# Performance work log

Measured on AMD Instinct MI355X. Metric: run time of the kernel, lower is better.

## Reference

```python
import jax, jax.numpy as jnp
import numpy as np

N_NODES = 100000
N_EDGES = 3200000
N_GRAPHS = 1000

def setup_inputs() -> dict:
    key = jax.random.key(0)
    ks = jax.random.split(key, 8)
    x = jax.random.normal(ks[0], (N_NODES, 4), dtype=jnp.float32)
    edge_index = jax.random.randint(ks[1], (2, N_EDGES), 0, N_NODES, dtype=jnp.int64)
    batch = jnp.sort(jax.random.randint(ks[2], (N_NODES,), 0, N_GRAPHS, dtype=jnp.int64))
    def glorot(k, shape):
        lim = np.sqrt(6.0 / (shape[0] + shape[1]))
        return jax.random.uniform(k, shape, jnp.float32, -lim, lim)
    return {
        'x': x, 'edge_index': edge_index, 'batch': batch,
        'W1': glorot(ks[3], (4, 16)),  'b1': jnp.zeros((16,), jnp.float32),
        'W2': glorot(ks[4], (16, 16)), 'b2': jnp.zeros((16,), jnp.float32),
        'W3': glorot(ks[5], (16, 16)), 'b3': jnp.zeros((16,), jnp.float32),
        'lin_w': glorot(ks[6], (16, 1)), 'lin_b': jnp.zeros((1,), jnp.float32),
    }

def _gcn_norm(edge_index, num_nodes):
    # PyG GCNConv default: add self-loops, symmetric normalization
    loop = jnp.arange(num_nodes, dtype=edge_index.dtype)
    row = jnp.concatenate([edge_index[0], loop])  # source
    col = jnp.concatenate([edge_index[1], loop])  # target
    ones = jnp.ones(row.shape[0], dtype=jnp.float32)
    deg = jax.ops.segment_sum(ones, col, num_segments=num_nodes)
    dinv = jnp.where(deg > 0, jax.lax.rsqrt(deg), 0.0)
    norm = dinv[row] * dinv[col]  # [E+N]
    return row, col, norm

def _gcn_conv(x, row, col, norm, W, b, num_nodes):
    h = x @ W                                   # small GEMM first (fewer msg bytes)
    msg = h[row] * norm[:, None]                # gather + scale
    out = jax.ops.segment_sum(msg, col, num_segments=num_nodes)  # scatter-add
    return out + b

def reference(x, edge_index, batch, W1, b1, W2, b2, W3, b3, lin_w, lin_b):
    n = x.shape[0]
    row, col, norm = _gcn_norm(edge_index, n)
    h = _gcn_conv(x, row, col, norm, W1, b1, n)
    h = _gcn_conv(h, row, col, norm, W2, b2, n)
    h = _gcn_conv(h, row, col, norm, W3, b3, n)
    # global_mean_pool
    sums = jax.ops.segment_sum(h, batch, num_segments=N_GRAPHS)
    cnt = jax.ops.segment_sum(jnp.ones((n,), jnp.float32), batch, num_segments=N_GRAPHS)
    pooled = sums / jnp.maximum(cnt, 1.0)[:, None]
    # dropout p=0.5 is identity in eval mode
    logits = pooled @ lin_w + lin_b
    return jax.nn.sigmoid(logits)
```

## Files before the change

kernel.cpp:

```cpp
#include <hip/hip_runtime.h>
#include <math.h>


#define SHIFT      8
#define BSZ        256
#define NB_SCAT    128
#define B_SCAT     256
#define B_GATH     512
#define ROWMASK    0x1FFFFu
#define PSLOTS     64

__global__ void hist_kernel(const int* __restrict__ col, int E, int tile, int nbuck,
                            unsigned* __restrict__ M,
                            const float* __restrict__ W1, const float* __restrict__ b1,
                            const float* __restrict__ W2, const float* __restrict__ b2,
                            const float* __restrict__ W3, const float* __restrict__ b3,
                            const float* __restrict__ lin_w, const float* __restrict__ lin_b,
                            float* __restrict__ coeff,
                            float* __restrict__ sums, float* __restrict__ cnt, int ngraphs) {
    extern __shared__ unsigned h[];
    __shared__ float w3l[16], w2l[16];
    int t = threadIdx.x;
    for (int i = t; i < nbuck; i += blockDim.x) h[i] = 0;
    if (blockIdx.x == 0) {
        for (int i = t; i < ngraphs; i += blockDim.x) { sums[i] = 0.f; cnt[i] = 0.f; }
        if (t < 16) {
            float s = 0.f;
            for (int j = 0; j < 16; ++j) s += W3[t * 16 + j] * lin_w[j];
            w3l[t] = s;
        }
    }
    __syncthreads();
    if (blockIdx.x == 0 && t < 16) {
        float s = 0.f;
        for (int j = 0; j < 16; ++j) s += W2[t * 16 + j] * w3l[j];
        w2l[t] = s;
    }
    __syncthreads();
    if (blockIdx.x == 0) {
        if (t < 4) {
            float s = 0.f;
            for (int j = 0; j < 16; ++j) s += W1[t * 16 + j] * w2l[j];
            coeff[t] = s;
        } else if (t == 4) {
            float s = 0.f;
            for (int j = 0; j < 16; ++j) s += b1[j] * w2l[j];
            coeff[4] = s;
        } else if (t == 5) {
            float s = 0.f;
            for (int j = 0; j < 16; ++j) s += b2[j] * w3l[j];
            coeff[5] = s;
        } else if (t == 6) {
            float s = 0.f;
            for (int j = 0; j < 16; ++j) s += b3[j] * lin_w[j];
            coeff[6] = s;
        } else if (t == 7) {
            coeff[7] = lin_b[0];
        }
    }
    int b = blockIdx.x;
    int s = b * tile, e = min(s + tile, E);
    if (s < e) {
        int nq = (e - s) >> 2;
        const int4* c4 = (const int4*)(col + s);
        for (int q = t; q < nq; q += blockDim.x) {
            int4 c = c4[q];
            atomicAdd(&h[((unsigned)c.x) >> SHIFT], 1u);
            atomicAdd(&h[((unsigned)c.y) >> SHIFT], 1u);
            atomicAdd(&h[((unsigned)c.z) >> SHIFT], 1u);
            atomicAdd(&h[((unsigned)c.w) >> SHIFT], 1u);
        }
        for (int k = s + (nq << 2) + t; k < e; k += blockDim.x)
            atomicAdd(&h[((unsigned)col[k]) >> SHIFT], 1u);
    }
    __syncthreads();
    for (int i = t; i < nbuck; i += blockDim.x)
        M[(size_t)b * nbuck + i] = h[i];
}

__global__ void scanA_kernel(unsigned* __restrict__ M, unsigned* __restrict__ binTotal,
                             int nbuck) {
    __shared__ unsigned sc[NB_SCAT];
    int b = blockIdx.x;
    int t = threadIdx.x;
    unsigned v = M[(size_t)t * nbuck + b];
    sc[t] = v;
    __syncthreads();
    for (int off = 1; off < NB_SCAT; off <<= 1) {
        unsigned u = (t >= off) ? sc[t - off] : 0u;
        __syncthreads();
        sc[t] += u;
        __syncthreads();
    }
    M[(size_t)t * nbuck + b] = sc[t] - v;
    if (t == NB_SCAT - 1) binTotal[b] = sc[t];
}

__global__ void scatter_kernel(const int* __restrict__ row, const int* __restrict__ col,
                               int E, int tile, int nbuck,
                               const unsigned* __restrict__ M,
                               const unsigned* __restrict__ binTotal,
                               unsigned* __restrict__ bstart,
                               unsigned* __restrict__ out) {
    extern __shared__ unsigned lds[];
    unsigned* bb   = lds;
    unsigned* base = lds + nbuck;
    unsigned* tsum = lds + 2 * nbuck;
    int t = threadIdx.x;
    const int C = (2048 + B_SCAT - 1) / B_SCAT;
    unsigned lv[C];
    unsigned ls = 0;
    for (int k = 0; k < C; ++k) {
        int i = t * C + k;
        unsigned x = (i < nbuck) ? binTotal[i] : 0u;
        lv[k] = ls; ls += x;
    }
    tsum[t] = ls;
    __syncthreads();
    for (int off = 1; off < B_SCAT; off <<= 1) {
        unsigned u = (t >= off) ? tsum[t - off] : 0u;
        __syncthreads();
        tsum[t] += u;
        __syncthreads();
    }
    unsigned ex = (t == 0) ? 0u : tsum[t - 1];
    for (int k = 0; k < C; ++k) {
        int i = t * C + k;
        if (i < nbuck) bb[i] = ex + lv[k];
    }
    __syncthreads();
    int j = blockIdx.x;
    for (int i = t; i < nbuck; i += blockDim.x)
        base[i] = bb[i] + M[(size_t)j * nbuck + i];
    if (j == 0) {
        for (int i = t; i < nbuck; i += blockDim.x) bstart[i] = bb[i];
        if (t == 0) bstart[nbuck] = (unsigned)E;
    }
    __syncthreads();
    int s = j * tile, e = min(s + tile, E);
    if (s < e) {
        int nq = (e - s) >> 2;
        const int4* r4 = (const int4*)(row + s);
        const int4* c4 = (const int4*)(col + s);
        for (int q = t; q < nq; q += blockDim.x) {
            int4 r = r4[q];
            int4 c = c4[q];
            unsigned p0 = atomicAdd(&base[((unsigned)c.x) >> SHIFT], 1u);
            unsigned p1 = atomicAdd(&base[((unsigned)c.y) >> SHIFT], 1u);
            unsigned p2 = atomicAdd(&base[((unsigned)c.z) >> SHIFT], 1u);
            unsigned p3 = atomicAdd(&base[((unsigned)c.w) >> SHIFT], 1u);
            out[p0] = (unsigned)r.x | (((unsigned)c.x & (BSZ - 1)) << 17);
            out[p1] = (unsigned)r.y | (((unsigned)c.y & (BSZ - 1)) << 17);
            out[p2] = (unsigned)r.z | (((unsigned)c.z & (BSZ - 1)) << 17);
            out[p3] = (unsigned)r.w | (((unsigned)c.w & (BSZ - 1)) << 17);
        }
        for (int k = s + (nq << 2) + t; k < e; k += blockDim.x) {
            unsigned c = (unsigned)col[k];
            unsigned pos = atomicAdd(&base[c >> SHIFT], 1u);
            out[pos] = (unsigned)row[k] | ((c & (BSZ - 1)) << 17);
        }
    }
}

__global__ void degnode0_kernel(const unsigned* __restrict__ buck,
                                const unsigned* __restrict__ bstart,
                                const float* __restrict__ x, const float* __restrict__ coeff,
                                float* __restrict__ dinv, float* __restrict__ g, int n) {
    __shared__ float acc[BSZ];
    int b = blockIdx.x;
    if (threadIdx.x < BSZ) acc[threadIdx.x] = 0.f;
    __syncthreads();
    unsigned s = bstart[b], e = bstart[b + 1];
    unsigned sa = (s + 3u) & ~3u;
    if (sa > e) sa = e;
    if (s + threadIdx.x < sa)
        atomicAdd(&acc[buck[s + threadIdx.x] >> 17], 1.0f);
    unsigned nq = (e - sa) >> 2;
    const uint4* bq = (const uint4*)(buck + sa);
    for (unsigned q = threadIdx.x; q < nq; q += blockDim.x) {
        uint4 w = bq[q];
        atomicAdd(&acc[w.x >> 17], 1.0f);
        atomicAdd(&acc[w.y >> 17], 1.0f);
        atomicAdd(&acc[w.z >> 17], 1.0f);
        atomicAdd(&acc[w.w >> 17], 1.0f);
    }
    for (unsigned k = sa + (nq << 2) + threadIdx.x; k < e; k += blockDim.x)
        atomicAdd(&acc[buck[k] >> 17], 1.0f);
    __syncthreads();
    int node = b * BSZ + threadIdx.x;
    if (threadIdx.x < BSZ && node < n) {
        float d = rsqrtf(acc[threadIdx.x] + 1.0f);
        dinv[node] = d;
        float4 xv = ((const float4*)x)[node];
        float t0 = xv.x * coeff[0] + xv.y * coeff[1] + xv.z * coeff[2] + xv.w * coeff[3];
        g[node] = d * t0;
    }
}

__global__ void gather_kernel(const unsigned* __restrict__ buck,
                              const unsigned* __restrict__ bstart,
                              const float* __restrict__ dinv, const float* __restrict__ gin,
                              float* __restrict__ gout, const float* __restrict__ coeff,
                              int sidx, int n) {
    __shared__ float acc[BSZ];
    int b = blockIdx.x;
    if (threadIdx.x < BSZ) acc[threadIdx.x] = 0.f;
    __syncthreads();
    unsigned s = bstart[b], e = bstart[b + 1];
    unsigned sa = (s + 3u) & ~3u;
    if (sa > e) sa = e;
    if (s + threadIdx.x < sa) {
        unsigned w = buck[s + threadIdx.x];
        atomicAdd(&acc[w >> 17], gin[w & ROWMASK]);
    }
    unsigned nq = (e - sa) >> 2;
    const uint4* bq = (const uint4*)(buck + sa);
    for (unsigned q = threadIdx.x; q < nq; q += blockDim.x) {
        uint4 w = bq[q];
        float a0 = gin[w.x & ROWMASK];
        float a1 = gin[w.y & ROWMASK];
        float a2 = gin[w.z & ROWMASK];
        float a3 = gin[w.w & ROWMASK];
        atomicAdd(&acc[w.x >> 17], a0);
        atomicAdd(&acc[w.y >> 17], a1);
        atomicAdd(&acc[w.z >> 17], a2);
        atomicAdd(&acc[w.w >> 17], a3);
    }
    for (unsigned k = sa + (nq << 2) + threadIdx.x; k < e; k += blockDim.x) {
        unsigned w = buck[k];
        atomicAdd(&acc[w >> 17], gin[w & ROWMASK]);
    }
    __syncthreads();
    int node = b * BSZ + threadIdx.x;
    if (threadIdx.x < BSZ && node < n) {
        float d = dinv[node];
        float t = d * (acc[threadIdx.x] + gin[node]) + coeff[sidx];
        gout[node] = d * t;
    }
}

__global__ void gatherpool_kernel(const unsigned* __restrict__ buck,
                                  const unsigned* __restrict__ bstart,
                                  const float* __restrict__ dinv, const float* __restrict__ gin,
                                  const float* __restrict__ coeff, const int* __restrict__ batch,
                                  float* __restrict__ sums, float* __restrict__ cnt, int n) {
    __shared__ float acc[BSZ];
    __shared__ float ls[PSLOTS], lc[PSLOTS];
    __shared__ int bF;
    int b = blockIdx.x;
    if (threadIdx.x < BSZ) acc[threadIdx.x] = 0.f;
    for (int i = threadIdx.x; i < PSLOTS; i += blockDim.x) { ls[i] = 0.f; lc[i] = 0.f; }
    if (threadIdx.x == 0) bF = batch[min(b * BSZ, n - 1)];
    __syncthreads();
    unsigned s = bstart[b], e = bstart[b + 1];
    unsigned sa = (s + 3u) & ~3u;
    if (sa > e) sa = e;
    if (s + threadIdx.x < sa) {
        unsigned w = buck[s + threadIdx.x];
        atomicAdd(&acc[w >> 17], gin[w & ROWMASK]);
    }
    unsigned nq = (e - sa) >> 2;
    const uint4* bq = (const uint4*)(buck + sa);
    for (unsigned q = threadIdx.x; q < nq; q += blockDim.x) {
        uint4 w = bq[q];
        float a0 = gin[w.x & ROWMASK];
        float a1 = gin[w.y & ROWMASK];
        float a2 = gin[w.z & ROWMASK];
        float a3 = gin[w.w & ROWMASK];
        atomicAdd(&acc[w.x >> 17], a0);
        atomicAdd(&acc[w.y >> 17], a1);
        atomicAdd(&acc[w.z >> 17], a2);
        atomicAdd(&acc[w.w >> 17], a3);
    }
    for (unsigned k = sa + (nq << 2) + threadIdx.x; k < e; k += blockDim.x) {
        unsigned w = buck[k];
        atomicAdd(&acc[w >> 17], gin[w & ROWMASK]);
    }
    __syncthreads();
    int node = b * BSZ + threadIdx.x;
    if (threadIdx.x < BSZ && node < n) {
        float d = dinv[node];
        float t3 = d * (acc[threadIdx.x] + gin[node]) + coeff[6];
        int rb = batch[node] - bF;
        if (rb < PSLOTS) {
            atomicAdd(&ls[rb], t3);
            atomicAdd(&lc[rb], 1.0f);
        } else {
            atomicAdd(&sums[bF + rb], t3);
            atomicAdd(&cnt[bF + rb], 1.0f);
        }
    }
    __syncthreads();
    for (int i = threadIdx.x; i < PSLOTS; i += blockDim.x) {
        if (lc[i] != 0.f) {
            atomicAdd(&sums[bF + i], ls[i]);
            atomicAdd(&cnt[bF + i], lc[i]);
        }
    }
}

__global__ void final_kernel(const float* __restrict__ sums, const float* __restrict__ cnt,
                             const float* __restrict__ coeff, float* __restrict__ out,
                             int ngraphs) {
    int i = blockIdx.x * blockDim.x + threadIdx.x;
    if (i < ngraphs) {
        float m = sums[i] / fmaxf(cnt[i], 1.0f) + coeff[7];
        out[i] = 1.0f / (1.0f + expf(-m));
    }
}

__global__ void fb_coeffs_kernel(const float* __restrict__ W1, const float* __restrict__ b1,
                                 const float* __restrict__ W2, const float* __restrict__ b2,
                                 const float* __restrict__ W3, const float* __restrict__ b3,
                                 const float* __restrict__ lin_w, const float* __restrict__ lin_b,
                                 float* __restrict__ coeff,
                                 float* __restrict__ sums, float* __restrict__ cnt, int ngraphs) {
    for (int i = threadIdx.x; i < ngraphs; i += blockDim.x) { sums[i] = 0.f; cnt[i] = 0.f; }
    if (threadIdx.x == 0) {
        float w3l[16], w2l[16];
        for (int i = 0; i < 16; ++i) {
            float s = 0.f;
            for (int j = 0; j < 16; ++j) s += W3[i * 16 + j] * lin_w[j];
            w3l[i] = s;
        }
        for (int i = 0; i < 16; ++i) {
            float s = 0.f;
            for (int j = 0; j < 16; ++j) s += W2[i * 16 + j] * w3l[j];
            w2l[i] = s;
        }
        for (int i = 0; i < 4; ++i) {
            float s = 0.f;
            for (int j = 0; j < 16; ++j) s += W1[i * 16 + j] * w2l[j];
            coeff[i] = s;
        }
        float s2 = 0.f, s1 = 0.f, s0 = 0.f;
        for (int j = 0; j < 16; ++j) {
            s2 += b1[j] * w2l[j];
            s1 += b2[j] * w3l[j];
            s0 += b3[j] * lin_w[j];
        }
        coeff[4] = s2; coeff[5] = s1; coeff[6] = s0; coeff[7] = lin_b[0];
    }
}
__global__ void fb_init_kernel(float* __restrict__ deg, int n) {
    int i = blockIdx.x * blockDim.x + threadIdx.x;
    int stride = gridDim.x * blockDim.x;
    for (int k = i; k < n; k += stride) deg[k] = 1.0f;
}
__global__ void fb_deg_kernel(const int* __restrict__ col, float* __restrict__ deg, int E) {
    int i = blockIdx.x * blockDim.x + threadIdx.x;
    int stride = gridDim.x * blockDim.x;
    for (int k = i; k < E; k += stride) atomicAdd(&deg[col[k]], 1.0f);
}
__global__ void fb_node0_kernel(const float* __restrict__ x, const float* __restrict__ coeff,
                                float* __restrict__ deg_dinv, float* __restrict__ g,
                                float* __restrict__ acc, int n) {
    int i = blockIdx.x * blockDim.x + threadIdx.x;
    int stride = gridDim.x * blockDim.x;
    for (int k = i; k < n; k += stride) {
        float d = rsqrtf(deg_dinv[k]);
        deg_dinv[k] = d;
        float4 xv = ((const float4*)x)[k];
        float t0 = xv.x * coeff[0] + xv.y * coeff[1] + xv.z * coeff[2] + xv.w * coeff[3];
        g[k] = d * t0;
        acc[k] = 0.f;
    }
}
__global__ void fb_edge_kernel(const int* __restrict__ ei, const float* __restrict__ g,
                               float* __restrict__ acc, int E) {
    int i = blockIdx.x * blockDim.x + threadIdx.x;
    int stride = gridDim.x * blockDim.x;
    for (int k = i; k < E; k += stride) atomicAdd(&acc[ei[E + k]], g[ei[k]]);
}
__global__ void fb_node_kernel(const float* __restrict__ dinv, float* __restrict__ g,
                               float* __restrict__ acc, const float* __restrict__ coeff,
                               int sidx, int n) {
    int i = blockIdx.x * blockDim.x + threadIdx.x;
    int stride = gridDim.x * blockDim.x;
    for (int k = i; k < n; k += stride) {
        float d = dinv[k];
        float t = d * (acc[k] + g[k]) + coeff[sidx];
        g[k] = d * t;
        acc[k] = 0.f;
    }
}
__global__ void fb_pool_kernel(const float* __restrict__ dinv, const float* __restrict__ g,
                               const float* __restrict__ acc, const float* __restrict__ coeff,
                               const int* __restrict__ batch, float* __restrict__ sums,
                               float* __restrict__ cnt, int n) {
    int i = blockIdx.x * blockDim.x + threadIdx.x;
    int stride = gridDim.x * blockDim.x;
    for (int k = i; k < n; k += stride) {
        float d = dinv[k];
        float t3 = d * (acc[k] + g[k]) + coeff[6];
        int b = batch[k];
        atomicAdd(&sums[b], t3);
        atomicAdd(&cnt[b], 1.0f);
    }
}

extern "C" void kernel_launch(void* const* d_in, const int* in_sizes, int n_in,
                              void* d_out, int out_size, void* d_ws, size_t ws_size,
                              hipStream_t stream) {
    const float* x     = (const float*)d_in[0];
    const int*   ei    = (const int*)d_in[1];
    const int*   batch = (const int*)d_in[2];
    const float* W1    = (const float*)d_in[3];
    const float* b1    = (const float*)d_in[4];
    const float* W2    = (const float*)d_in[5];
    const float* b2    = (const float*)d_in[6];
    const float* W3    = (const float*)d_in[7];
    const float* b3    = (const float*)d_in[8];
    const float* lin_w = (const float*)d_in[9];
    const float* lin_b = (const float*)d_in[10];

    const int n       = in_sizes[0] / 4;
    const int E       = in_sizes[1] / 2;
    const int ngraphs = out_size;

    const int nbuck = (n + BSZ - 1) / BSZ;
    const int B = 256;

    size_t npad  = ((size_t)n + 255) & ~(size_t)255;
    size_t gpad  = ((size_t)ngraphs + 255) & ~(size_t)255;
    size_t nbpad = ((size_t)nbuck + 1 + 255) & ~(size_t)255;
    size_t mlen  = (size_t)NB_SCAT * nbuck;

    size_t need = (256 + mlen + 2 * nbpad + (size_t)E + 3 * npad + 2 * gpad) * 4;

    float* ws    = (float*)d_ws;
    float* coeff = ws;
    unsigned* M        = (unsigned*)(coeff + 256);
    unsigned* binTotal = M + mlen;
    unsigned* bstart   = binTotal + nbpad;
    unsigned* buck     = bstart + nbpad;
    float* dinv  = (float*)(buck + E);
    float* gA    = dinv + npad;
    float* gB    = gA + npad;
    float* sums  = gB + npad;
    float* cnt   = sums + gpad;

    bool mainok = (n < (1 << 17)) && nbuck >= 1 && nbuck <= 2048 && ws_size >= need;

    if (!mainok) {
        float* fcoeff = ws;
        float* deg = fcoeff + 256;
        float* g   = deg + npad;
        float* acc = g + npad;
        float* fsums = acc + npad;
        float* fcnt  = fsums + gpad;
        int nodeBlocks = (n + B - 1) / B;
        int edgeBlocks = (E + B - 1) / B;
        fb_coeffs_kernel<<<1, 64, 0, stream>>>(W1, b1, W2, b2, W3, b3, lin_w, lin_b, fcoeff,
                                               fsums, fcnt, ngraphs);
        fb_init_kernel<<<nodeBlocks, B, 0, stream>>>(deg, n);
        fb_deg_kernel<<<edgeBlocks, B, 0, stream>>>(ei + E, deg, E);
        fb_node0_kernel<<<nodeBlocks, B, 0, stream>>>(x, fcoeff, deg, g, acc, n);
        fb_edge_kernel<<<edgeBlocks, B, 0, stream>>>(ei, g, acc, E);
        fb_node_kernel<<<nodeBlocks, B, 0, stream>>>(deg, g, acc, fcoeff, 4, n);
        fb_edge_kernel<<<edgeBlocks, B, 0, stream>>>(ei, g, acc, E);
        fb_node_kernel<<<nodeBlocks, B, 0, stream>>>(deg, g, acc, fcoeff, 5, n);
        fb_edge_kernel<<<edgeBlocks, B, 0, stream>>>(ei, g, acc, E);
        fb_pool_kernel<<<nodeBlocks, B, 0, stream>>>(deg, g, acc, fcoeff, batch, fsums, fcnt, n);
        final_kernel<<<(ngraphs + B - 1) / B, B, 0, stream>>>(fsums, fcnt, fcoeff, (float*)d_out, ngraphs);
        return;
    }

    int tile = (((E + NB_SCAT - 1) / NB_SCAT) + 3) & ~3;
    size_t ldsHist = (size_t)nbuck * sizeof(unsigned);
    size_t ldsScat = (size_t)(2 * nbuck + B_SCAT) * sizeof(unsigned);

    hist_kernel<<<NB_SCAT, B_SCAT, ldsHist, stream>>>(ei + E, E, tile, nbuck, M,
                                                      W1, b1, W2, b2, W3, b3, lin_w, lin_b,
                                                      coeff, sums, cnt, ngraphs);
    scanA_kernel<<<nbuck, NB_SCAT, 0, stream>>>(M, binTotal, nbuck);
    scatter_kernel<<<NB_SCAT, B_SCAT, ldsScat, stream>>>(ei, ei + E, E, tile, nbuck, M,
                                                         binTotal, bstart, buck);

    degnode0_kernel<<<nbuck, B_GATH, 0, stream>>>(buck, bstart, x, coeff, dinv, gA, n);
    gather_kernel<<<nbuck, B_GATH, 0, stream>>>(buck, bstart, dinv, gA, gB, coeff, 4, n);
    gather_kernel<<<nbuck, B_GATH, 0, stream>>>(buck, bstart, dinv, gB, gA, coeff, 5, n);
    gatherpool_kernel<<<nbuck, B_GATH, 0, stream>>>(buck, bstart, dinv, gA, coeff, batch,
                                                    sums, cnt, n);

    final_kernel<<<(ngraphs + B - 1) / B, B, 0, stream>>>(sums, cnt, coeff, (float*)d_out, ngraphs);
}
```

Measured before the change: 149.9 us.

## Stage edge scatter in LDS and write buckets out coalesced

```diff
diff --git a/kernel.cpp b/kernel.cpp
--- a/kernel.cpp
+++ b/kernel.cpp
@@ -4,11 +4,12 @@
 
 #define SHIFT      8
 #define BSZ        256
-#define NB_SCAT    128
+#define NB_SCAT    256
 #define B_SCAT     256
 #define B_GATH     512
 #define ROWMASK    0x1FFFFu
 #define PSLOTS     64
+#define MAXNB      2048
 
 __global__ void hist_kernel(const int* __restrict__ col, int E, int tile, int nbuck,
                             unsigned* __restrict__ M,
@@ -103,41 +104,81 @@
                                unsigned* __restrict__ bstart,
                                unsigned* __restrict__ out) {
     extern __shared__ unsigned lds[];
-    unsigned* bb   = lds;
-    unsigned* base = lds + nbuck;
-    unsigned* tsum = lds + 2 * nbuck;
-    int t = threadIdx.x;
-    const int C = (2048 + B_SCAT - 1) / B_SCAT;
+    unsigned* h     = lds;
+    unsigned* lofs  = lds + nbuck;
+    unsigned* lcur  = lds + 2 * nbuck;
+    unsigned* gbase = lds + 3 * nbuck;
+    unsigned* tsum  = lds + 4 * nbuck;
+    unsigned* stage = lds + 4 * nbuck + B_SCAT;
+    int t = threadIdx.x, j = blockIdx.x;
+    for (int i = t; i < nbuck; i += blockDim.x) h[i] = 0;
+    __syncthreads();
+    int s = j * tile, e = min(s + tile, E);
+    if (s < e) {
+        int nq = (e - s) >> 2;
+        const int4* c4 = (const int4*)(col + s);
+        for (int q = t; q < nq; q += blockDim.x) {
+            int4 c = c4[q];
+            atomicAdd(&h[((unsigned)c.x) >> SHIFT], 1u);
+            atomicAdd(&h[((unsigned)c.y) >> SHIFT], 1u);
+            atomicAdd(&h[((unsigned)c.z) >> SHIFT], 1u);
+            atomicAdd(&h[((unsigned)c.w) >> SHIFT], 1u);
+        }
+        for (int k = s + (nq << 2) + t; k < e; k += blockDim.x)
+            atomicAdd(&h[((unsigned)col[k]) >> SHIFT], 1u);
+    }
+    __syncthreads();
+    const int C = MAXNB / B_SCAT;
     unsigned lv[C];
-    unsigned ls = 0;
-    for (int k = 0; k < C; ++k) {
-        int i = t * C + k;
-        unsigned x = (i < nbuck) ? binTotal[i] : 0u;
-        lv[k] = ls; ls += x;
-    }
-    tsum[t] = ls;
-    __syncthreads();
-    for (int off = 1; off < B_SCAT; off <<= 1) {
-        unsigned u = (t >= off) ? tsum[t - off] : 0u;
+    {
+        unsigned run = 0;
+        for (int k = 0; k < C; ++k) {
+            int i = t * C + k;
+            unsigned x = (i < nbuck) ? h[i] : 0u;
+            lv[k] = run; run += x;
+        }
+        tsum[t] = run;
         __syncthreads();
-        tsum[t] += u;
+        for (int off = 1; off < B_SCAT; off <<= 1) {
+            unsigned u = (t >= off) ? tsum[t - off] : 0u;
+            __syncthreads();
+            tsum[t] += u;
+            __syncthreads();
+        }
+        unsigned ex = (t == 0) ? 0u : tsum[t - 1];
+        for (int k = 0; k < C; ++k) {
+            int i = t * C + k;
+            if (i < nbuck) { lofs[i] = ex + lv[k]; lcur[i] = ex + lv[k]; }
+        }
+    }
+    __syncthreads();
+    {
+        unsigned run = 0;
+        for (int k = 0; k < C; ++k) {
+            int i = t * C + k;
+            unsigned x = (i < nbuck) ? binTotal[i] : 0u;
+            lv[k] = run; run += x;
+        }
+        tsum[t] = run;
         __syncthreads();
-    }
-    unsigned ex = (t == 0) ? 0u : tsum[t - 1];
-    for (int k = 0; k < C; ++k) {
-        int i = t * C + k;
-        if (i < nbuck) bb[i] = ex + lv[k];
-    }
-    __syncthreads();
-    int j = blockIdx.x;
-    for (int i = t; i < nbuck; i += blockDim.x)
-        base[i] = bb[i] + M[(size_t)j * nbuck + i];
-    if (j == 0) {
-        for (int i = t; i < nbuck; i += blockDim.x) bstart[i] = bb[i];
-        if (t == 0) bstart[nbuck] = (unsigned)E;
-    }
-    __syncthreads();
-    int s = j * tile, e = min(s + tile, E);
+        for (int off = 1; off < B_SCAT; off <<= 1) {
+            unsigned u = (t >= off) ? tsum[t - off] : 0u;
+            __syncthreads();
+            tsum[t] += u;
+            __syncthreads();
+        }
+        unsigned ex = (t == 0) ? 0u : tsum[t - 1];
+        for (int k = 0; k < C; ++k) {
+            int i = t * C + k;
+            if (i < nbuck) {
+                unsigned bb = ex + lv[k];
+                gbase[i] = bb + M[(size_t)j * nbuck + i];
+                if (j == 0) bstart[i] = bb;
+            }
+        }
+        if (j == 0 && t == 0) bstart[nbuck] = (unsigned)E;
+    }
+    __syncthreads();
     if (s < e) {
         int nq = (e - s) >> 2;
         const int4* r4 = (const int4*)(row + s);
@@ -145,20 +186,27 @@
         for (int q = t; q < nq; q += blockDim.x) {
             int4 r = r4[q];
             int4 c = c4[q];
-            unsigned p0 = atomicAdd(&base[((unsigned)c.x) >> SHIFT], 1u);
-            unsigned p1 = atomicAdd(&base[((unsigned)c.y) >> SHIFT], 1u);
-            unsigned p2 = atomicAdd(&base[((unsigned)c.z) >> SHIFT], 1u);
-            unsigned p3 = atomicAdd(&base[((unsigned)c.w) >> SHIFT], 1u);
-            out[p0] = (unsigned)r.x | (((unsigned)c.x & (BSZ - 1)) << 17);
-            out[p1] = (unsigned)r.y | (((unsigned)c.y & (BSZ - 1)) << 17);
-            out[p2] = (unsigned)r.z | (((unsigned)c.z & (BSZ - 1)) << 17);
-            out[p3] = (unsigned)r.w | (((unsigned)c.w & (BSZ - 1)) << 17);
+            unsigned p0 = atomicAdd(&lcur[((unsigned)c.x) >> SHIFT], 1u);
+            unsigned p1 = atomicAdd(&lcur[((unsigned)c.y) >> SHIFT], 1u);
+            unsigned p2 = atomicAdd(&lcur[((unsigned)c.z) >> SHIFT], 1u);
+            unsigned p3 = atomicAdd(&lcur[((unsigned)c.w) >> SHIFT], 1u);
+            stage[p0] = (unsigned)r.x | (((unsigned)c.x & (BSZ - 1)) << 17);
+            stage[p1] = (unsigned)r.y | (((unsigned)c.y & (BSZ - 1)) << 17);
+            stage[p2] = (unsigned)r.z | (((unsigned)c.z & (BSZ - 1)) << 17);
+            stage[p3] = (unsigned)r.w | (((unsigned)c.w & (BSZ - 1)) << 17);
         }
         for (int k = s + (nq << 2) + t; k < e; k += blockDim.x) {
             unsigned c = (unsigned)col[k];
-            unsigned pos = atomicAdd(&base[c >> SHIFT], 1u);
-            out[pos] = (unsigned)row[k] | ((c & (BSZ - 1)) << 17);
-        }
+            unsigned pos = atomicAdd(&lcur[c >> SHIFT], 1u);
+            stage[pos] = (unsigned)row[k] | ((c & (BSZ - 1)) << 17);
+        }
+    }
+    __syncthreads();
+    int wid = t >> 6, lane = t & 63, nw = blockDim.x >> 6;
+    for (int b = wid; b < nbuck; b += nw) {
+        unsigned cntb = h[b], lo = lofs[b], go = gbase[b];
+        for (unsigned i = lane; i < cntb; i += 64)
+            out[go + i] = stage[lo + i];
     }
 }
 
@@ -440,7 +488,11 @@
     float* sums  = gB + npad;
     float* cnt   = sums + gpad;
 
-    bool mainok = (n < (1 << 17)) && nbuck >= 1 && nbuck <= 2048 && ws_size >= need;
+    int tile = (((E + NB_SCAT - 1) / NB_SCAT) + 3) & ~3;
+    size_t ldsScat = (size_t)(4 * nbuck + B_SCAT + tile) * sizeof(unsigned);
+
+    bool mainok = (n < (1 << 17)) && nbuck >= 1 && nbuck <= MAXNB &&
+                  ws_size >= need && ldsScat <= 63 * 1024;
 
     if (!mainok) {
         float* fcoeff = ws;
@@ -466,9 +518,7 @@
         return;
     }
 
-    int tile = (((E + NB_SCAT - 1) / NB_SCAT) + 3) & ~3;
     size_t ldsHist = (size_t)nbuck * sizeof(unsigned);
-    size_t ldsScat = (size_t)(2 * nbuck + B_SCAT) * sizeof(unsigned);
 
     hist_kernel<<<NB_SCAT, B_SCAT, ldsHist, stream>>>(ei + E, E, tile, nbuck, M,
                                                       W1, b1, W2, b2, W3, b3, lin_w, lin_b,
```

Measured after the change: 146.6 us. 1.02x faster.
